# Performance work log

Measured on AMD Instinct MI355X. Metric: run time of the kernel, lower is better.

The kernel has to match this reference:

```python
import jax, jax.numpy as jnp
import numpy as np

B, C, H = 32768, 1000, 128


def setup_inputs() -> dict:
    key = jax.random.key(0)
    ks = jax.random.split(key, 4)
    return {
        "logits": jax.random.normal(ks[0], (B, C), dtype=jnp.float32),
        "W1": jax.random.normal(ks[1], (C, H), dtype=jnp.float32) * 0.02,
        "b1": jnp.zeros((H,), dtype=jnp.float32),
        "W2": jax.random.normal(ks[2], (H, H), dtype=jnp.float32) * 0.02,
        "b2": jnp.zeros((H,), dtype=jnp.float32),
        "W3": jax.random.normal(ks[3], (H, C), dtype=jnp.float32) * 0.02,
        "b3": jnp.zeros((C,), dtype=jnp.float32),
    }


def reference(logits, W1, b1, W2, b2, W3, b3):
    prob = jax.nn.softmax(logits, axis=-1)                      # [B, C]
    # descending sort (torch.sort(descending=True))
    order = jnp.argsort(-prob, axis=-1)                          # [B, C] int
    sorted_prob = jnp.take_along_axis(prob, order, axis=-1)      # [B, C]
    # diffs between consecutive sorted probs, last slot = 1
    diffs = jnp.concatenate(
        [sorted_prob[:, :-1] - sorted_prob[:, 1:],
         jnp.ones((prob.shape[0], 1), dtype=prob.dtype)], axis=1)
    # adapter MLP on prob
    h = jax.nn.relu(prob @ W1 + b1)
    h = jax.nn.relu(h @ W2 + b2)
    cal = h @ W3 + b3                                            # [B, C]
    # sigmoid on all but the last column
    cal = jnp.concatenate([jax.nn.sigmoid(cal[:, :-1]), cal[:, -1:]], axis=1)
    v = diffs * cal                                              # [B, C]
    # S.T @ U @ v  ==  scatter(reverse-cumsum(v)) back to original order
    rev_cumsum = jnp.cumsum(v[:, ::-1], axis=1)[:, ::-1]         # suffix sum
    rows = jnp.arange(logits.shape[0])[:, None]
    fitted = jnp.zeros_like(logits).at[rows, order].set(rev_cumsum)
    return fitted + logits
```

## Files before the change

### kernel.cpp

```cpp
#include <hip/hip_runtime.h>
#include <hip/hip_bf16.h>

#define BROWS 32768
#define CDIM 1000
#define CPAD 1024
#define HDIM 128
#define SWZ(w) ((w) ^ ((((w) >> 5) & 7) << 2))

typedef __attribute__((ext_vector_type(8))) short short8;
typedef __attribute__((ext_vector_type(4))) float f32x4;

__device__ inline unsigned short f2bf(float x) {
    unsigned int b = __float_as_uint(x);
    unsigned int r = (b + 0x7FFFu + ((b >> 16) & 1u)) >> 16;
    return (unsigned short)r;
}
__device__ inline float bf2f(unsigned short u) {
    return __uint_as_float(((unsigned int)u) << 16);
}

__global__ __launch_bounds__(256) void k_prep(const float* __restrict__ W1,
                                              const float* __restrict__ W2,
                                              const float* __restrict__ W3,
                                              unsigned short* __restrict__ W1t,
                                              unsigned short* __restrict__ W2t,
                                              unsigned short* __restrict__ W3t) {
    const int idx = blockIdx.x * 256 + threadIdx.x;
    {
        const int n = idx >> 10, k = idx & 1023;
        W1t[idx] = (k < CDIM) ? f2bf(W1[(size_t)k * HDIM + n]) : (unsigned short)0;
    }
    {
        const int n = idx >> 7, k = idx & 127;
        W3t[idx] = (n < CDIM) ? f2bf(W3[(size_t)k * CDIM + n]) : (unsigned short)0;
    }
    if (idx < 16384) {
        const int n = idx >> 7, k = idx & 127;
        W2t[idx] = f2bf(W2[(size_t)k * HDIM + n]);
    }
}

__global__ __launch_bounds__(256) void k_softmax(const float* __restrict__ logits,
                                                 unsigned short* __restrict__ prob) {
    const int wv = threadIdx.x >> 6, lane = threadIdx.x & 63;
    const int row = (blockIdx.x << 2) + wv;
    const int base = lane << 4;
    const float* lrow = logits + (size_t)row * CDIM;
    float lg[16];
#pragma unroll
    for (int q = 0; q < 4; ++q) {
        const int c = base + (q << 2);
        if (c < CDIM) {
            const float4 v4 = *reinterpret_cast<const float4*>(lrow + c);
            lg[q * 4] = v4.x; lg[q * 4 + 1] = v4.y; lg[q * 4 + 2] = v4.z; lg[q * 4 + 3] = v4.w;
        } else {
            lg[q * 4] = lg[q * 4 + 1] = lg[q * 4 + 2] = lg[q * 4 + 3] = -INFINITY;
        }
    }
    float mx = lg[0];
#pragma unroll
    for (int e = 1; e < 16; ++e) mx = fmaxf(mx, lg[e]);
#pragma unroll
    for (int off = 32; off >= 1; off >>= 1) mx = fmaxf(mx, __shfl_xor(mx, off));
    float p[16], s = 0.f;
#pragma unroll
    for (int e = 0; e < 16; ++e) { p[e] = __expf(lg[e] - mx); s += p[e]; }
#pragma unroll
    for (int off = 32; off >= 1; off >>= 1) s += __shfl_xor(s, off);
    const float inv = 1.f / s;
    unsigned int w[8];
#pragma unroll
    for (int i = 0; i < 8; ++i) {
        const unsigned int lo = f2bf(p[2 * i] * inv);
        const unsigned int hi = f2bf(p[2 * i + 1] * inv);
        w[i] = lo | (hi << 16);
    }
    uint4 o0, o1;
    o0.x = w[0]; o0.y = w[1]; o0.z = w[2]; o0.w = w[3];
    o1.x = w[4]; o1.y = w[5]; o1.z = w[6]; o1.w = w[7];
    uint4* dst = reinterpret_cast<uint4*>(prob + (size_t)row * CPAD + base);
    dst[0] = o0; dst[1] = o1;
}

template <int EPI>
__global__ __launch_bounds__(512) void k_gemm(const unsigned short* __restrict__ A, int lda,
                                              const unsigned short* __restrict__ Bt, int ldb,
                                              const float* __restrict__ bias,
                                              unsigned short* __restrict__ outp, int ldo,
                                              int K, int nlimit) {
    __shared__ uint4 As[128 * 8];
    __shared__ uint4 Bs[128 * 8];
    const int tid = threadIdx.x;
    const int bm = blockIdx.x, bn = blockIdx.y;
    const int lane = tid & 63, w = tid >> 6;
    const int wm = (w >> 1) << 5;
    const int wn = (w & 1) << 6;
    const int l15 = lane & 15, l4 = lane >> 4;
    f32x4 acc[2][4] = {};

    for (int k0 = 0; k0 < K; k0 += 64) {
        __syncthreads();
#pragma unroll
        for (int i = 0; i < 2; ++i) {
            const int cid = tid + (i << 9);
            const int r = cid >> 3, c = cid & 7;
            As[(r << 3) + (c ^ (r & 7))] =
                *reinterpret_cast<const uint4*>(A + (size_t)(bm * 128 + r) * lda + k0 + (c << 3));
            Bs[(r << 3) + (c ^ (r & 7))] =
                *reinterpret_cast<const uint4*>(Bt + (size_t)(bn * 128 + r) * ldb + k0 + (c << 3));
        }
        __syncthreads();
#pragma unroll
        for (int kk = 0; kk < 2; ++kk) {
            short8 a[2], b[4];
#pragma unroll
            for (int mf = 0; mf < 2; ++mf) {
                const int r = wm + (mf << 4) + l15;
                a[mf] = *reinterpret_cast<const short8*>(&As[(r << 3) + (((kk << 2) + l4) ^ (r & 7))]);
            }
#pragma unroll
            for (int nf = 0; nf < 4; ++nf) {
                const int r = wn + (nf << 4) + l15;
                b[nf] = *reinterpret_cast<const short8*>(&Bs[(r << 3) + (((kk << 2) + l4) ^ (r & 7))]);
            }
#pragma unroll
            for (int mf = 0; mf < 2; ++mf)
#pragma unroll
                for (int nf = 0; nf < 4; ++nf)
                    acc[mf][nf] = __builtin_amdgcn_mfma_f32_16x16x32_bf16(a[mf], b[nf], acc[mf][nf], 0, 0, 0);
        }
    }
#pragma unroll
    for (int mf = 0; mf < 2; ++mf) {
#pragma unroll
        for (int nf = 0; nf < 4; ++nf) {
            const int n = (bn << 7) + wn + (nf << 4) + l15;
            if (EPI == 1 && n >= nlimit) continue;
            const float bv = bias[n];
#pragma unroll
            for (int r = 0; r < 4; ++r) {
                const int m = (bm << 7) + wm + (mf << 4) + (l4 << 2) + r;
                float v = acc[mf][nf][r] + bv;
                if (EPI == 0) {
                    v = fmaxf(v, 0.f);
                } else {
                    if (n != nlimit - 1) v = 1.f / (1.f + __expf(-v));
                }
                outp[(size_t)m * ldo + n] = f2bf(v);
            }
        }
    }
}

__global__ __launch_bounds__(256) void k_sortfinish(const float* __restrict__ logits,
                                                    const unsigned short* __restrict__ cal,
                                                    float* __restrict__ out) {
    __shared__ unsigned int shm[4 * 1024];
    const int wv = threadIdx.x >> 6, lane = threadIdx.x & 63;
    const int row = (blockIdx.x << 2) + wv;
    unsigned int* sm = &shm[wv << 10];
    const int base = lane << 4;

    int cb[4];
#pragma unroll
    for (int j = 0; j < 4; ++j) { const int wd = base + (j << 2); cb[j] = SWZ(wd); }

    {
        uint4 z; z.x = 0; z.y = 0; z.z = 0; z.w = 0;
#pragma unroll
        for (int j = 0; j < 4; ++j) *reinterpret_cast<uint4*>(&sm[cb[j]]) = z;
    }

    const float* lrow = logits + (size_t)row * CDIM;
    float lg[16];
#pragma unroll
    for (int q = 0; q < 4; ++q) {
        const int c = base + (q << 2);
        if (c < CDIM) {
            const float4 v4 = *reinterpret_cast<const float4*>(lrow + c);
            lg[q * 4] = v4.x; lg[q * 4 + 1] = v4.y; lg[q * 4 + 2] = v4.z; lg[q * 4 + 3] = v4.w;
        } else {
            lg[q * 4] = lg[q * 4 + 1] = lg[q * 4 + 2] = lg[q * 4 + 3] = -INFINITY;
        }
    }
    const unsigned short* crow = cal + (size_t)row * CDIM + base;
    const uint4 c0v = *reinterpret_cast<const uint4*>(crow);
    const uint4 c1v = *reinterpret_cast<const uint4*>(crow + 8);

    float mx = lg[0];
#pragma unroll
    for (int e = 1; e < 16; ++e) mx = fmaxf(mx, lg[e]);
#pragma unroll
    for (int off = 32; off >= 1; off >>= 1) mx = fmaxf(mx, __shfl_xor(mx, off));
    float p[16], s = 0.f;
#pragma unroll
    for (int e = 0; e < 16; ++e) { p[e] = __expf(lg[e] - mx); s += p[e]; }
#pragma unroll
    for (int off = 32; off >= 1; off >>= 1) s += __shfl_xor(s, off);
    const float inv = 1.f / s;
#pragma unroll
    for (int e = 0; e < 16; ++e) p[e] *= inv;

    unsigned int offv[16]; int swk[16];
#pragma unroll
    for (int e = 0; e < 16; ++e) {
        const unsigned int key = __float_as_uint(p[e]) >> 20;
        swk[e] = SWZ((int)key);
        offv[e] = (base + e < CDIM) ? atomicAdd(&sm[swk[e]], 1u) : 0u;
    }

    {
        unsigned int c16[16];
#pragma unroll
        for (int j = 0; j < 4; ++j) {
            const uint4 v4 = *reinterpret_cast<const uint4*>(&sm[cb[j]]);
            c16[4 * j] = v4.x; c16[4 * j + 1] = v4.y; c16[4 * j + 2] = v4.z; c16[4 * j + 3] = v4.w;
        }
        unsigned int lsum = 0;
#pragma unroll
        for (int e = 0; e < 16; ++e) lsum += c16[e];
        unsigned int suf = lsum;
#pragma unroll
        for (int off = 1; off < 64; off <<= 1) {
            const unsigned int u = __shfl_down(suf, off);
            if (lane + off < 64) suf += u;
        }
        unsigned int run = suf - lsum;
        unsigned int stv[16];
#pragma unroll
        for (int e = 15; e >= 0; --e) { stv[e] = run; run += c16[e]; }
#pragma unroll
        for (int j = 0; j < 4; ++j) {
            uint4 v4;
            v4.x = stv[4 * j]; v4.y = stv[4 * j + 1]; v4.z = stv[4 * j + 2]; v4.w = stv[4 * j + 3];
            *reinterpret_cast<uint4*>(&sm[cb[j]]) = v4;
        }
    }

    int swr[16];
#pragma unroll
    for (int e = 0; e < 16; ++e) {
        const int rk = (base + e < CDIM) ? (int)(sm[swk[e]] + offv[e]) : 1023;
        swr[e] = SWZ(rk);
    }

#pragma unroll
    for (int e = 0; e < 16; ++e)
        if (base + e < CDIM) sm[swr[e]] = __float_as_uint(p[e]);

    float sp[16];
#pragma unroll
    for (int j = 0; j < 4; ++j) {
        const uint4 v4 = *reinterpret_cast<const uint4*>(&sm[cb[j]]);
        sp[4 * j] = __uint_as_float(v4.x); sp[4 * j + 1] = __uint_as_float(v4.y);
        sp[4 * j + 2] = __uint_as_float(v4.z); sp[4 * j + 3] = __uint_as_float(v4.w);
    }
    const float spn_next = __shfl_down(sp[0], 1);
    const unsigned int cw[8] = {c0v.x, c0v.y, c0v.z, c0v.w, c1v.x, c1v.y, c1v.z, c1v.w};
    float v[16];
#pragma unroll
    for (int e = 0; e < 16; ++e) {
        const int r = base + e;
        const float cv = bf2f((unsigned short)((cw[e >> 1] >> ((e & 1) * 16)) & 0xFFFFu));
        const float spn = (e < 15) ? sp[e + 1] : spn_next;
        float val;
        if (r < CDIM - 1) val = (sp[e] - spn) * cv;
        else if (r == CDIM - 1) val = cv;
        else val = 0.f;
        v[e] = val;
    }
    float lsuf[16], run = 0.f;
#pragma unroll
    for (int e = 15; e >= 0; --e) { run += v[e]; lsuf[e] = run; }
    float pi = run;
#pragma unroll
    for (int off = 1; off < 64; off <<= 1) {
        const float u = __shfl_up(pi, off);
        if (lane >= off) pi += u;
    }
    const float tot = __shfl(pi, 63);
    const float after = tot - pi;

#pragma unroll
    for (int j = 0; j < 4; ++j) {
        uint4 v4;
        v4.x = __float_as_uint(lsuf[4 * j] + after);
        v4.y = __float_as_uint(lsuf[4 * j + 1] + after);
        v4.z = __float_as_uint(lsuf[4 * j + 2] + after);
        v4.w = __float_as_uint(lsuf[4 * j + 3] + after);
        *reinterpret_cast<uint4*>(&sm[cb[j]]) = v4;
    }
    float f[16];
#pragma unroll
    for (int e = 0; e < 16; ++e) f[e] = __uint_as_float(sm[swr[e]]);
#pragma unroll
    for (int q = 0; q < 4; ++q) {
        const int c = base + (q << 2);
        if (c < CDIM) {
            float4 o;
            o.x = lg[q * 4] + f[q * 4];
            o.y = lg[q * 4 + 1] + f[q * 4 + 1];
            o.z = lg[q * 4 + 2] + f[q * 4 + 2];
            o.w = lg[q * 4 + 3] + f[q * 4 + 3];
            *reinterpret_cast<float4*>(out + (size_t)row * CDIM + c) = o;
        }
    }
}

extern "C" void kernel_launch(void* const* d_in, const int* in_sizes, int n_in,
                              void* d_out, int out_size, void* d_ws, size_t ws_size,
                              hipStream_t stream) {
    const float* logits = (const float*)d_in[0];
    const float* W1 = (const float*)d_in[1];
    const float* b1 = (const float*)d_in[2];
    const float* W2 = (const float*)d_in[3];
    const float* b2 = (const float*)d_in[4];
    const float* W3 = (const float*)d_in[5];
    const float* b3 = (const float*)d_in[6];
    float* out = (float*)d_out;

    char* ws = (char*)d_ws;
    unsigned short* prob = (unsigned short*)ws;
    unsigned short* h1   = (unsigned short*)(ws + 67108864);
    unsigned short* h2   = (unsigned short*)(ws + 75497472);
    unsigned short* W1t  = (unsigned short*)(ws + 83886080);
    unsigned short* W2t  = (unsigned short*)(ws + 84148224);
    unsigned short* W3t  = (unsigned short*)(ws + 84180992);
    unsigned short* cal  = prob;

    k_prep<<<512, 256, 0, stream>>>(W1, W2, W3, W1t, W2t, W3t);
    k_softmax<<<BROWS / 4, 256, 0, stream>>>(logits, prob);
    k_gemm<0><<<dim3(BROWS / 128, 1), 512, 0, stream>>>(prob, CPAD, W1t, CPAD, b1, h1, HDIM, CPAD, 0);
    k_gemm<0><<<dim3(BROWS / 128, 1), 512, 0, stream>>>(h1, HDIM, W2t, HDIM, b2, h2, HDIM, HDIM, 0);
    k_gemm<1><<<dim3(BROWS / 128, 8), 512, 0, stream>>>(h2, HDIM, W3t, HDIM, b3, cal, CDIM, HDIM, CDIM);
    k_sortfinish<<<BROWS / 4, 256, 0, stream>>>(logits, cal, out);
}
```

Baseline: 177.5 us.

## Reuse softmax row stats in sort kernel and process two rows per wave

The softmax kernel now writes each row's max and inverse sum to a small workspace array. The sort/finish kernel reads these instead of redoing the max and sum wave reductions. Each wave now handles two rows with interleaved independent work, to expose more instruction-level parallelism. The h1 and h2 buffers are merged, so the second GEMM runs in place. The cost is double the LDS per block and higher register pressure, which can lower occupancy, and the in-place GEMM relies on each block reading its A rows before writing them.

```diff
diff --git a/kernel.cpp b/kernel.cpp
--- a/kernel.cpp
+++ b/kernel.cpp
@@ -41,7 +41,8 @@
 }
 
 __global__ __launch_bounds__(256) void k_softmax(const float* __restrict__ logits,
-                                                 unsigned short* __restrict__ prob) {
+                                                 unsigned short* __restrict__ prob,
+                                                 float2* __restrict__ rstat) {
     const int wv = threadIdx.x >> 6, lane = threadIdx.x & 63;
     const int row = (blockIdx.x << 2) + wv;
     const int base = lane << 4;
@@ -80,6 +81,7 @@
     o1.x = w[4]; o1.y = w[5]; o1.z = w[6]; o1.w = w[7];
     uint4* dst = reinterpret_cast<uint4*>(prob + (size_t)row * CPAD + base);
     dst[0] = o0; dst[1] = o1;
+    if (lane == 0) rstat[row] = make_float2(mx, inv);
 }
 
 template <int EPI>
@@ -153,67 +155,73 @@
 }
 
 __global__ __launch_bounds__(256) void k_sortfinish(const float* __restrict__ logits,
+                                                    const float2* __restrict__ rstat,
                                                     const unsigned short* __restrict__ cal,
                                                     float* __restrict__ out) {
-    __shared__ unsigned int shm[4 * 1024];
+    __shared__ unsigned int shm[8 * 1024];
     const int wv = threadIdx.x >> 6, lane = threadIdx.x & 63;
-    const int row = (blockIdx.x << 2) + wv;
-    unsigned int* sm = &shm[wv << 10];
     const int base = lane << 4;
+    const int row0 = (blockIdx.x << 3) + (wv << 1);
+    unsigned int* const smx[2] = { &shm[wv << 11], &shm[(wv << 11) + 1024] };
 
     int cb[4];
 #pragma unroll
-    for (int j = 0; j < 4; ++j) { const int wd = base + (j << 2); cb[j] = SWZ(wd); }
+    for (int j = 0; j < 4; ++j) cb[j] = SWZ(base + (j << 2));
+
+    float lg[2][16]; unsigned int cw[2][8]; float mxv[2], invv[2];
+#pragma unroll
+    for (int h = 0; h < 2; ++h) {
+        const int row = row0 + h;
+        const float* lrow = logits + (size_t)row * CDIM;
+#pragma unroll
+        for (int q = 0; q < 4; ++q) {
+            const int c = base + (q << 2);
+            if (c < CDIM) {
+                const float4 v4 = *reinterpret_cast<const float4*>(lrow + c);
+                lg[h][q * 4] = v4.x; lg[h][q * 4 + 1] = v4.y;
+                lg[h][q * 4 + 2] = v4.z; lg[h][q * 4 + 3] = v4.w;
+            } else {
+                lg[h][q * 4] = lg[h][q * 4 + 1] = lg[h][q * 4 + 2] = lg[h][q * 4 + 3] = -INFINITY;
+            }
+        }
+        const unsigned short* crow = cal + (size_t)row * CDIM + base;
+        const uint4 c0 = *reinterpret_cast<const uint4*>(crow);
+        const uint4 c1 = *reinterpret_cast<const uint4*>(crow + 8);
+        cw[h][0] = c0.x; cw[h][1] = c0.y; cw[h][2] = c0.z; cw[h][3] = c0.w;
+        cw[h][4] = c1.x; cw[h][5] = c1.y; cw[h][6] = c1.z; cw[h][7] = c1.w;
+        const float2 st = rstat[row];
+        mxv[h] = st.x; invv[h] = st.y;
+    }
 
     {
         uint4 z; z.x = 0; z.y = 0; z.z = 0; z.w = 0;
 #pragma unroll
-        for (int j = 0; j < 4; ++j) *reinterpret_cast<uint4*>(&sm[cb[j]]) = z;
-    }
-
-    const float* lrow = logits + (size_t)row * CDIM;
-    float lg[16];
-#pragma unroll
-    for (int q = 0; q < 4; ++q) {
-        const int c = base + (q << 2);
-        if (c < CDIM) {
-            const float4 v4 = *reinterpret_cast<const float4*>(lrow + c);
-            lg[q * 4] = v4.x; lg[q * 4 + 1] = v4.y; lg[q * 4 + 2] = v4.z; lg[q * 4 + 3] = v4.w;
-        } else {
-            lg[q * 4] = lg[q * 4 + 1] = lg[q * 4 + 2] = lg[q * 4 + 3] = -INFINITY;
-        }
-    }
-    const unsigned short* crow = cal + (size_t)row * CDIM + base;
-    const uint4 c0v = *reinterpret_cast<const uint4*>(crow);
-    const uint4 c1v = *reinterpret_cast<const uint4*>(crow + 8);
-
-    float mx = lg[0];
-#pragma unroll
-    for (int e = 1; e < 16; ++e) mx = fmaxf(mx, lg[e]);
-#pragma unroll
-    for (int off = 32; off >= 1; off >>= 1) mx = fmaxf(mx, __shfl_xor(mx, off));
-    float p[16], s = 0.f;
-#pragma unroll
-    for (int e = 0; e < 16; ++e) { p[e] = __expf(lg[e] - mx); s += p[e]; }
-#pragma unroll
-    for (int off = 32; off >= 1; off >>= 1) s += __shfl_xor(s, off);
-    const float inv = 1.f / s;
-#pragma unroll
-    for (int e = 0; e < 16; ++e) p[e] *= inv;
-
-    unsigned int offv[16]; int swk[16];
-#pragma unroll
-    for (int e = 0; e < 16; ++e) {
-        const unsigned int key = __float_as_uint(p[e]) >> 20;
-        swk[e] = SWZ((int)key);
-        offv[e] = (base + e < CDIM) ? atomicAdd(&sm[swk[e]], 1u) : 0u;
-    }
-
-    {
+        for (int h = 0; h < 2; ++h)
+#pragma unroll
+            for (int j = 0; j < 4; ++j) *reinterpret_cast<uint4*>(&smx[h][cb[j]]) = z;
+    }
+
+    float p[2][16];
+#pragma unroll
+    for (int h = 0; h < 2; ++h)
+#pragma unroll
+        for (int e = 0; e < 16; ++e) p[h][e] = __expf(lg[h][e] - mxv[h]) * invv[h];
+
+    unsigned int offv[2][16];
+#pragma unroll
+    for (int h = 0; h < 2; ++h)
+#pragma unroll
+        for (int e = 0; e < 16; ++e) {
+            const unsigned int key = __float_as_uint(p[h][e]) >> 20;
+            offv[h][e] = (base + e < CDIM) ? atomicAdd(&smx[h][SWZ((int)key)], 1u) : 0u;
+        }
+
+#pragma unroll
+    for (int h = 0; h < 2; ++h) {
         unsigned int c16[16];
 #pragma unroll
         for (int j = 0; j < 4; ++j) {
-            const uint4 v4 = *reinterpret_cast<const uint4*>(&sm[cb[j]]);
+            const uint4 v4 = *reinterpret_cast<const uint4*>(&smx[h][cb[j]]);
             c16[4 * j] = v4.x; c16[4 * j + 1] = v4.y; c16[4 * j + 2] = v4.z; c16[4 * j + 3] = v4.w;
         }
         unsigned int lsum = 0;
@@ -233,78 +241,96 @@
         for (int j = 0; j < 4; ++j) {
             uint4 v4;
             v4.x = stv[4 * j]; v4.y = stv[4 * j + 1]; v4.z = stv[4 * j + 2]; v4.w = stv[4 * j + 3];
-            *reinterpret_cast<uint4*>(&sm[cb[j]]) = v4;
-        }
-    }
-
-    int swr[16];
-#pragma unroll
-    for (int e = 0; e < 16; ++e) {
-        const int rk = (base + e < CDIM) ? (int)(sm[swk[e]] + offv[e]) : 1023;
-        swr[e] = SWZ(rk);
-    }
-
-#pragma unroll
-    for (int e = 0; e < 16; ++e)
-        if (base + e < CDIM) sm[swr[e]] = __float_as_uint(p[e]);
-
-    float sp[16];
-#pragma unroll
-    for (int j = 0; j < 4; ++j) {
-        const uint4 v4 = *reinterpret_cast<const uint4*>(&sm[cb[j]]);
-        sp[4 * j] = __uint_as_float(v4.x); sp[4 * j + 1] = __uint_as_float(v4.y);
-        sp[4 * j + 2] = __uint_as_float(v4.z); sp[4 * j + 3] = __uint_as_float(v4.w);
-    }
-    const float spn_next = __shfl_down(sp[0], 1);
-    const unsigned int cw[8] = {c0v.x, c0v.y, c0v.z, c0v.w, c1v.x, c1v.y, c1v.z, c1v.w};
-    float v[16];
-#pragma unroll
-    for (int e = 0; e < 16; ++e) {
-        const int r = base + e;
-        const float cv = bf2f((unsigned short)((cw[e >> 1] >> ((e & 1) * 16)) & 0xFFFFu));
-        const float spn = (e < 15) ? sp[e + 1] : spn_next;
-        float val;
-        if (r < CDIM - 1) val = (sp[e] - spn) * cv;
-        else if (r == CDIM - 1) val = cv;
-        else val = 0.f;
-        v[e] = val;
-    }
-    float lsuf[16], run = 0.f;
-#pragma unroll
-    for (int e = 15; e >= 0; --e) { run += v[e]; lsuf[e] = run; }
-    float pi = run;
-#pragma unroll
-    for (int off = 1; off < 64; off <<= 1) {
-        const float u = __shfl_up(pi, off);
-        if (lane >= off) pi += u;
-    }
-    const float tot = __shfl(pi, 63);
-    const float after = tot - pi;
-
-#pragma unroll
-    for (int j = 0; j < 4; ++j) {
-        uint4 v4;
-        v4.x = __float_as_uint(lsuf[4 * j] + after);
-        v4.y = __float_as_uint(lsuf[4 * j + 1] + after);
-        v4.z = __float_as_uint(lsuf[4 * j + 2] + after);
-        v4.w = __float_as_uint(lsuf[4 * j + 3] + after);
-        *reinterpret_cast<uint4*>(&sm[cb[j]]) = v4;
-    }
-    float f[16];
-#pragma unroll
-    for (int e = 0; e < 16; ++e) f[e] = __uint_as_float(sm[swr[e]]);
-#pragma unroll
-    for (int q = 0; q < 4; ++q) {
-        const int c = base + (q << 2);
-        if (c < CDIM) {
-            float4 o;
-            o.x = lg[q * 4] + f[q * 4];
-            o.y = lg[q * 4 + 1] + f[q * 4 + 1];
-            o.z = lg[q * 4 + 2] + f[q * 4 + 2];
-            o.w = lg[q * 4 + 3] + f[q * 4 + 3];
-            *reinterpret_cast<float4*>(out + (size_t)row * CDIM + c) = o;
-        }
-    }
+            *reinterpret_cast<uint4*>(&smx[h][cb[j]]) = v4;
+        }
+    }
+
+    int swr[2][16];
+#pragma unroll
+    for (int h = 0; h < 2; ++h)
+#pragma unroll
+        for (int e = 0; e < 16; ++e) {
+            const unsigned int key = __float_as_uint(p[h][e]) >> 20;
+            const int rk = (base + e < CDIM) ? (int)(smx[h][SWZ((int)key)] + offv[h][e]) : 1023;
+            swr[h][e] = SWZ(rk);
+        }
+
+#pragma unroll
+    for (int h = 0; h < 2; ++h)
+#pragma unroll
+        for (int e = 0; e < 16; ++e)
+            if (base + e < CDIM) smx[h][swr[h][e]] = __float_as_uint(p[h][e]);
+
+    float sp[2][16];
+#pragma unroll
+    for (int h = 0; h < 2; ++h)
+#pragma unroll
+        for (int j = 0; j < 4; ++j) {
+            const uint4 v4 = *reinterpret_cast<const uint4*>(&smx[h][cb[j]]);
+            sp[h][4 * j] = __uint_as_float(v4.x); sp[h][4 * j + 1] = __uint_as_float(v4.y);
+            sp[h][4 * j + 2] = __uint_as_float(v4.z); sp[h][4 * j + 3] = __uint_as_float(v4.w);
+        }
+
+    float lsuf[2][16], after[2];
+#pragma unroll
+    for (int h = 0; h < 2; ++h) {
+        const float spn_next = __shfl_down(sp[h][0], 1);
+        float v[16];
+#pragma unroll
+        for (int e = 0; e < 16; ++e) {
+            const int r = base + e;
+            const float cv = bf2f((unsigned short)((cw[h][e >> 1] >> ((e & 1) * 16)) & 0xFFFFu));
+            const float spn = (e < 15) ? sp[h][e + 1] : spn_next;
+            float val;
+            if (r < CDIM - 1) val = (sp[h][e] - spn) * cv;
+            else if (r == CDIM - 1) val = cv;
+            else val = 0.f;
+            v[e] = val;
+        }
+        float run = 0.f;
+#pragma unroll
+        for (int e = 15; e >= 0; --e) { run += v[e]; lsuf[h][e] = run; }
+        float pi = run;
+#pragma unroll
+        for (int off = 1; off < 64; off <<= 1) {
+            const float u = __shfl_up(pi, off);
+            if (lane >= off) pi += u;
+        }
+        const float tot = __shfl(pi, 63);
+        after[h] = tot - pi;
+    }
+
+#pragma unroll
+    for (int h = 0; h < 2; ++h)
+#pragma unroll
+        for (int j = 0; j < 4; ++j) {
+            uint4 v4;
+            v4.x = __float_as_uint(lsuf[h][4 * j] + after[h]);
+            v4.y = __float_as_uint(lsuf[h][4 * j + 1] + after[h]);
+            v4.z = __float_as_uint(lsuf[h][4 * j + 2] + after[h]);
+            v4.w = __float_as_uint(lsuf[h][4 * j + 3] + after[h]);
+            *reinterpret_cast<uint4*>(&smx[h][cb[j]]) = v4;
+        }
+    float f[2][16];
+#pragma unroll
+    for (int h = 0; h < 2; ++h)
+#pragma unroll
+        for (int e = 0; e < 16; ++e) f[h][e] = __uint_as_float(smx[h][swr[h][e]]);
+
+#pragma unroll
+    for (int h = 0; h < 2; ++h)
+#pragma unroll
+        for (int q = 0; q < 4; ++q) {
+            const int c = base + (q << 2);
+            if (c < CDIM) {
+                float4 o;
+                o.x = lg[h][q * 4] + f[h][q * 4];
+                o.y = lg[h][q * 4 + 1] + f[h][q * 4 + 1];
+                o.z = lg[h][q * 4 + 2] + f[h][q * 4 + 2];
+                o.w = lg[h][q * 4 + 3] + f[h][q * 4 + 3];
+                *reinterpret_cast<float4*>(out + (size_t)(row0 + h) * CDIM + c) = o;
+            }
+        }
 }
 
 extern "C" void kernel_launch(void* const* d_in, const int* in_sizes, int n_in,
@@ -321,17 +347,17 @@
 
     char* ws = (char*)d_ws;
     unsigned short* prob = (unsigned short*)ws;
-    unsigned short* h1   = (unsigned short*)(ws + 67108864);
-    unsigned short* h2   = (unsigned short*)(ws + 75497472);
-    unsigned short* W1t  = (unsigned short*)(ws + 83886080);
-    unsigned short* W2t  = (unsigned short*)(ws + 84148224);
-    unsigned short* W3t  = (unsigned short*)(ws + 84180992);
+    unsigned short* h12  = (unsigned short*)(ws + 67108864);
+    float2*         rstat= (float2*)(ws + 75497472);
+    unsigned short* W1t  = (unsigned short*)(ws + 75759616);
+    unsigned short* W2t  = (unsigned short*)(ws + 76021760);
+    unsigned short* W3t  = (unsigned short*)(ws + 76054528);
     unsigned short* cal  = prob;
 
     k_prep<<<512, 256, 0, stream>>>(W1, W2, W3, W1t, W2t, W3t);
-    k_softmax<<<BROWS / 4, 256, 0, stream>>>(logits, prob);
-    k_gemm<0><<<dim3(BROWS / 128, 1), 512, 0, stream>>>(prob, CPAD, W1t, CPAD, b1, h1, HDIM, CPAD, 0);
-    k_gemm<0><<<dim3(BROWS / 128, 1), 512, 0, stream>>>(h1, HDIM, W2t, HDIM, b2, h2, HDIM, HDIM, 0);
-    k_gemm<1><<<dim3(BROWS / 128, 8), 512, 0, stream>>>(h2, HDIM, W3t, HDIM, b3, cal, CDIM, HDIM, CDIM);
-    k_sortfinish<<<BROWS / 4, 256, 0, stream>>>(logits, cal, out);
-}
+    k_softmax<<<BROWS / 4, 256, 0, stream>>>(logits, prob, rstat);
+    k_gemm<0><<<dim3(BROWS / 128, 1), 512, 0, stream>>>(prob, CPAD, W1t, CPAD, b1, h12, HDIM, CPAD, 0);
+    k_gemm<0><<<dim3(BROWS / 128, 1), 512, 0, stream>>>(h12, HDIM, W2t, HDIM, b2, h12, HDIM, HDIM, 0);
+    k_gemm<1><<<dim3(BROWS / 128, 8), 512, 0, stream>>>(h12, HDIM, W3t, HDIM, b3, cal, CDIM, HDIM, CDIM);
+    k_sortfinish<<<BROWS / 8, 256, 0, stream>>>(logits, rstat, cal, out);
+}
```

Result: slower. 185.6 us (+4.5%).
